# Optimization experiments

Hardware: AMD Instinct MI355X
Metric: run time of the kernel (lower is better)

Reference implementation:

```python
import jax, jax.numpy as jnp
import numpy as np

EPS = 1e-6       # eps from __init__
STEPSIZE = 1.0   # stepsize from __init__
DELTA = 0.1      # delta from __init__


def setup_inputs() -> dict:
    key = jax.random.key(0)
    k1, k2, k3 = jax.random.split(key, 3)
    N, L, H, E, M = 2, 2048, 8, 64, 64
    return {
        "queries": jax.random.normal(k1, (N, L, H, E), dtype=jnp.float32),
        "keys": jax.random.normal(k2, (N, L, H, E), dtype=jnp.float32),
        "values": jax.random.normal(k3, (N, L, H, M), dtype=jnp.float32),
        "key_lengths_mask": jnp.ones((N, L), dtype=jnp.float32),
    }


def reference(queries, keys, values, key_lengths_mask):
    # elu feature map: elu(x) + 1
    Q = jax.nn.elu(queries) + 1.0                                   # [N,L,H,E]
    K = (jax.nn.elu(keys) + 1.0) * key_lengths_mask[:, :, None, None]
    N, L, H, E = Q.shape

    # normalizer Z_t = 1 / (q_t . sum_{s<=t} k_s + eps)
    Z = 1.0 / (jnp.einsum('nlhe,nlhe->nlh', Q, jnp.cumsum(K, axis=1)) + EPS)

    # per-step outer products k_s v_s^T  (original materializes this einsum)
    KV = jnp.einsum('nlhe,nlhm->nlhem', K, values)                  # [N,L,H,E,M]

    # causal_dot_product: out_t = q_t . cumsum_s(KV)_t
    out = jnp.einsum('nlhe,nlhem->nlhm', Q, jnp.cumsum(KV, axis=1)) * Z[..., None]

    # momentum coefficients mu_j from Frobenius norms over (E,M)
    diff_norm = jnp.sqrt(jnp.sum((KV[:, 1:] - KV[:, :-1]) ** 2, axis=(3, 4)))  # [N,L-1,H]
    base_norm = jnp.sqrt(jnp.sum(KV[:, :-1] ** 2, axis=(3, 4)))
    mu = jnp.clip((1.0 - jnp.sqrt(diff_norm / base_norm)) ** 2, 0.0, 1.0 - DELTA)

    # momentum weights: a_{L-1}=1, a_j = 1 + mu_j * a_{j+1} (backward recurrence).
    # This equals both momentum_weight (cumprod-sum form) and momentum_weight_old
    # (explicit reverse loop) in the original, so Kn == Kw.
    def step(a, mu_t):
        a_new = 1.0 + mu_t * a
        return a_new, a_new

    _, a_seq = jax.lax.scan(step, jnp.ones((N, H), Q.dtype),
                            jnp.moveaxis(mu, 1, 0), reverse=True)   # [L-1,N,H]
    momentum_weight = jnp.concatenate(
        [jnp.moveaxis(a_seq, 0, 1), jnp.ones((N, 1, H), Q.dtype)], axis=1)  # [N,L,H]
    Kn = K * momentum_weight[..., None] * STEPSIZE                  # [N,L,H,E]

    return out, Kn
```

## Files before the change

### kernel.cpp

```cpp
#include <hip/hip_runtime.h>

#define N_ 2
#define L_ 2048
#define H_ 8
#define NH_ 16
#define C_ 64
#define NC_ 32
#define EPS_ 1e-6f
#define DELTA_ 0.1f

#define CHSZ 4160
#define ST_SHORTS (NH_*NC_*CHSZ)
#define KV_SHORTS (NH_*L_*64)

typedef short s8v __attribute__((ext_vector_type(8)));
typedef short s4v __attribute__((ext_vector_type(4)));
typedef float f4v __attribute__((ext_vector_type(4)));

__device__ __forceinline__ float elup1(float x){ return x>0.f ? x+1.f : __expf(x); }
__device__ __forceinline__ short f2b(float x){
  unsigned u = __float_as_uint(x);
  return (short)((u + 0x7FFFu + ((u>>16)&1u)) >> 16);
}
__device__ __forceinline__ float b2f(short s){
  return __uint_as_float(((unsigned)(unsigned short)s) << 16);
}

__global__ __launch_bounds__(512) void kA(const float* __restrict__ keys,
    const float* __restrict__ values, const float* __restrict__ mask,
    unsigned short* __restrict__ st, short* __restrict__ ktil,
    short* __restrict__ vtilT, float* __restrict__ mu)
{
  const int bid = blockIdx.x, c = bid & (NC_-1), nh = bid >> 5;
  const int n = nh >> 3, h = nh & 7, tid = threadIdx.x;

  __shared__ __attribute__((aligned(16))) short Ktb[64][72];
  __shared__ __attribute__((aligned(16))) short Vtb[80][72];
  __shared__ float prt[6][4][64];

  #pragma unroll
  for (int i = 0; i < 2; ++i) {
    const int idx4 = tid + 512*i;
    const int t = idx4 >> 4, e4 = (idx4 & 15) << 2;
    const int l = c*C_ + t;
    const size_t b = (((size_t)n*L_ + l)*H_ + h)*64 + e4;
    const float m0 = mask[n*L_ + l];
    const f4v kx = *(const f4v*)&keys[b];
    const f4v vx = *(const f4v*)&values[b];
    s4v kb4;
    #pragma unroll
    for (int j = 0; j < 4; ++j) kb4[j] = f2b(elup1(kx[j]) * m0);
    *(s4v*)&ktil[((size_t)nh*L_ + l)*64 + e4] = kb4;
    #pragma unroll
    for (int j = 0; j < 4; ++j) { Ktb[e4+j][t] = kb4[j]; Vtb[e4+j][t] = f2b(vx[j]); }
  }
  if (tid < 64) Vtb[64][tid] = (short)0x3F80;
  __syncthreads();

  {
    const int m = tid >> 3, t8 = (tid & 7) << 3;
    *(s8v*)&vtilT[((size_t)bid*64 + m)*64 + t8] = *(const s8v*)&Vtb[m][t8];
  }

  if (tid < 256) {
    const int lane = tid & 63, w = tid >> 6, r = lane & 15, g = lane >> 4;
    f4v acc[5];
    #pragma unroll
    for (int j = 0; j < 5; ++j) acc[j] = (f4v)(0.f);
    #pragma unroll
    for (int k2 = 0; k2 < 2; ++k2) {
      const s8v a = *(const s8v*)&Ktb[w*16 + r][k2*32 + g*8];
      #pragma unroll
      for (int mj = 0; mj < 5; ++mj) {
        const s8v bb = *(const s8v*)&Vtb[mj*16 + r][k2*32 + g*8];
        acc[mj] = __builtin_amdgcn_mfma_f32_16x16x32_bf16(a, bb, acc[mj], 0, 0, 0);
      }
    }
    unsigned short* sp = st + (size_t)bid*CHSZ;
    #pragma unroll
    for (int mj = 0; mj < 5; ++mj) {
      const int m = mj*16 + r;
      if (m <= 64) {
        s4v pk;
        #pragma unroll
        for (int j = 0; j < 4; ++j) pk[j] = f2b(acc[mj][j]);
        *(s4v*)&sp[(size_t)m*64 + w*16 + g*4] = pk;
      }
    }
  } else {
    const int tid2 = tid - 256;
    const int t = tid2 & 63, eq = tid2 >> 6;
    const int l = c*C_ + t;
    const int l1 = (l+1 < L_) ? l+1 : l;
    const size_t b0 = (((size_t)n*L_ + l )*H_ + h)*64 + eq*16;
    const size_t b1 = (((size_t)n*L_ + l1)*H_ + h)*64 + eq*16;
    const float m0 = mask[n*L_ + l], m1 = mask[n*L_ + l1];
    float kk0=0.f,kk1=0.f,knn=0.f,vv0=0.f,vv1=0.f,vnn=0.f;
    #pragma unroll
    for (int j = 0; j < 16; j += 4) {
      const f4v ka = *(const f4v*)&keys[b0+j];
      const f4v kc = *(const f4v*)&keys[b1+j];
      const f4v va = *(const f4v*)&values[b0+j];
      const f4v vc = *(const f4v*)&values[b1+j];
      #pragma unroll
      for (int jj = 0; jj < 4; ++jj) {
        const float k0 = elup1(ka[jj])*m0, k1 = elup1(kc[jj])*m1;
        kk0 += k0*k0; kk1 += k1*k1; knn += k0*k1;
        const float v0 = va[jj], v1 = vc[jj];
        vv0 += v0*v0; vv1 += v1*v1; vnn += v0*v1;
      }
    }
    prt[0][eq][t]=kk0; prt[1][eq][t]=kk1; prt[2][eq][t]=knn;
    prt[3][eq][t]=vv0; prt[4][eq][t]=vv1; prt[5][eq][t]=vnn;
  }
  __syncthreads();
  if (tid < 64) {
    float s[6];
    #pragma unroll
    for (int q2 = 0; q2 < 6; ++q2)
      s[q2] = prt[q2][0][tid]+prt[q2][1][tid]+prt[q2][2][tid]+prt[q2][3][tid];
    const int j = c*C_ + tid;
    float mval = 0.f;
    if (j < L_-1) {
      const float base2 = s[0]*s[3];
      float diff2 = s[1]*s[4] - 2.f*s[2]*s[5] + base2;
      diff2 = fmaxf(diff2, 0.f);
      if (base2 > 0.f) {
        const float r4 = sqrtf(sqrtf(diff2/base2));
        const float om = 1.f - r4;
        mval = fminf(om*om, 1.f - DELTA_);
      } else {
        mval = 1.f - DELTA_;
      }
    }
    mu[(size_t)nh*L_ + j] = mval;
  }
}

__global__ __launch_bounds__(256) void kBC(unsigned short* __restrict__ st,
    const float* __restrict__ mu, float* __restrict__ aw)
{
  const int bx = blockIdx.x, tid = threadIdx.x;
  if (bx < 260) {
    const int id = bx*256 + tid;
    const int nh2 = id / CHSZ;
    const int elem = id - nh2*CHSZ;
    unsigned short* base = st + (size_t)nh2*NC_*CHSZ + elem;
    unsigned short rr[NC_];
    #pragma unroll
    for (int c2 = 0; c2 < NC_; ++c2) rr[c2] = base[(size_t)c2*CHSZ];
    float acc = 0.f;
    #pragma unroll
    for (int c2 = 0; c2 < NC_; ++c2) {
      const float v = b2f((short)rr[c2]);
      base[(size_t)c2*CHSZ] = (unsigned short)f2b(acc);
      acc += v;
    }
    return;
  }
  const int nh2 = bx - 260;
  const float* mup = mu + (size_t)nh2*L_;
  float* awp = aw + (size_t)nh2*L_;
  __shared__ float Psc[256], Qsc[256];
  float lm[8];
  #pragma unroll
  for (int i = 0; i < 8; ++i) lm[i] = mup[tid*8 + i];
  float p = 1.f, q = 0.f;
  #pragma unroll
  for (int i = 7; i >= 0; --i) { q = lm[i]*q + 1.f; p *= lm[i]; }
  Psc[tid] = p; Qsc[tid] = q;
  __syncthreads();
  for (int d = 1; d < 256; d <<= 1) {
    float pr = 1.f, qr = 0.f;
    const bool has = (tid + d) < 256;
    if (has) { pr = Psc[tid+d]; qr = Qsc[tid+d]; }
    __syncthreads();
    if (has) { const float np = p*pr, nq = p*qr + q; p = np; q = nq; Psc[tid] = p; Qsc[tid] = q; }
    __syncthreads();
  }
  float x = (tid == 255) ? 1.f : Psc[tid+1] + Qsc[tid+1];
  #pragma unroll
  for (int i = 7; i >= 0; --i) { x = lm[i]*x + 1.f; awp[tid*8+i] = x; }
}

__global__ __launch_bounds__(512) void kD(const float* __restrict__ queries,
    const unsigned short* __restrict__ st, const short* __restrict__ ktil,
    const short* __restrict__ vtilT, const float* __restrict__ aw,
    float* __restrict__ out, float* __restrict__ kn)
{
  const int bid = blockIdx.x, c = bid & (NC_-1), nh = bid >> 5;
  const int n = nh >> 3, h = nh & 7, tid = threadIdx.x;
  const int lane = tid & 63, w = tid >> 6, r = lane & 15, g = lane >> 4;
  const int tt = w & 3, mg = w >> 2;

  __shared__ __attribute__((aligned(16))) short Qb[64][72];
  __shared__ __attribute__((aligned(16))) short Kb[64][72];
  __shared__ __attribute__((aligned(16))) union {
    short Pb[64][72];
    float outf[64][68];
  } U;
  __shared__ float Zl[64], al[64];

  const unsigned short* sp = st + (size_t)bid*CHSZ;
  const short* vp = vtilT + (size_t)bid*4096;
  const s8v zero8 = (s8v)(0);

  s8v sfrag[2][3], srow64[2];
  #pragma unroll
  for (int k2 = 0; k2 < 2; ++k2) {
    if (mg == 0) {
      #pragma unroll
      for (int mi = 0; mi < 3; ++mi)
        sfrag[k2][mi] = *(const s8v*)&sp[(size_t)(mi*16 + r)*64 + k2*32 + g*8];
      srow64[k2] = zero8;
    } else {
      sfrag[k2][0] = *(const s8v*)&sp[(size_t)(48 + r)*64 + k2*32 + g*8];
      srow64[k2] = (r == 0) ? *(const s8v*)&sp[(size_t)64*64 + k2*32 + g*8] : zero8;
      sfrag[k2][1] = zero8; sfrag[k2][2] = zero8;
    }
  }

  #pragma unroll
  for (int i = 0; i < 2; ++i) {
    const int idx4 = tid + 512*i;
    const int t = idx4 >> 4, e4 = (idx4 & 15) << 2;
    const int l = c*C_ + t;
    const f4v qx = __builtin_nontemporal_load(
        (const f4v*)&queries[(((size_t)n*L_ + l)*H_ + h)*64 + e4]);
    s4v qb4;
    #pragma unroll
    for (int j = 0; j < 4; ++j) qb4[j] = f2b(elup1(qx[j]));
    *(s4v*)&Qb[t][e4] = qb4;
  }
  {
    const int t = tid >> 3, e8 = (tid & 7) << 3;
    *(s8v*)&Kb[t][e8] = *(const s8v*)&ktil[((size_t)nh*L_ + c*C_ + t)*64 + e8];
  }
  if (tid < 64) al[tid] = aw[(size_t)nh*L_ + c*C_ + tid];
  __syncthreads();

  {
    const int ss = tt, th = mg;
    const bool live = (ss*16) <= (th*32 + 31);
    f4v pacc[2];
    pacc[0] = (f4v)(0.f); pacc[1] = (f4v)(0.f);
    if (live) {
      #pragma unroll
      for (int k2 = 0; k2 < 2; ++k2) {
        const s8v a = *(const s8v*)&Kb[ss*16 + r][k2*32 + g*8];
        #pragma unroll
        for (int tj2 = 0; tj2 < 2; ++tj2) {
          const s8v bb = *(const s8v*)&Qb[(th*2 + tj2)*16 + r][k2*32 + g*8];
          pacc[tj2] = __builtin_amdgcn_mfma_f32_16x16x32_bf16(a, bb, pacc[tj2], 0, 0, 0);
        }
      }
    }
    #pragma unroll
    for (int tj2 = 0; tj2 < 2; ++tj2) {
      const int t = (th*2 + tj2)*16 + r;
      s4v pk;
      #pragma unroll
      for (int j = 0; j < 4; ++j) {
        const int s2 = ss*16 + g*4 + j;
        pk[j] = (live && s2 <= t) ? f2b(pacc[tj2][j]) : (short)0;
      }
      *(s4v*)&U.Pb[t][ss*16 + g*4] = pk;
    }
  }

  s8v vfrag[2][3], vones;
  #pragma unroll
  for (int k2 = 0; k2 < 2; ++k2) {
    if (mg == 0) {
      #pragma unroll
      for (int mi = 0; mi < 3; ++mi)
        vfrag[k2][mi] = *(const s8v*)&vp[(size_t)(mi*16 + r)*64 + k2*32 + g*8];
    } else {
      vfrag[k2][0] = *(const s8v*)&vp[(size_t)(48 + r)*64 + k2*32 + g*8];
      vfrag[k2][1] = zero8; vfrag[k2][2] = zero8;
    }
  }
  {
    s8v o;
    #pragma unroll
    for (int j = 0; j < 8; ++j) o[j] = (short)0x3F80;
    vones = (r == 0 && mg == 1) ? o : zero8;
  }
  __syncthreads();

  const int nmj = (mg == 0) ? 3 : 2;
  f4v oacc[3];
  #pragma unroll
  for (int j = 0; j < 3; ++j) oacc[j] = (f4v)(0.f);
  #pragma unroll
  for (int k2 = 0; k2 < 4; ++k2) {
    const s8v a = (k2 < 2) ? *(const s8v*)&Qb[tt*16 + r][k2*32 + g*8]
                           : *(const s8v*)&U.Pb[tt*16 + r][(k2-2)*32 + g*8];
    #pragma unroll
    for (int mi = 0; mi < 3; ++mi) {
      if (mi < nmj) {
        s8v bb;
        if (k2 < 2) bb = (mg == 1 && mi == 1) ? srow64[k2] : sfrag[k2][mi];
        else        bb = (mg == 1 && mi == 1) ? vones      : vfrag[k2-2][mi];
        oacc[mi] = __builtin_amdgcn_mfma_f32_16x16x32_bf16(a, bb, oacc[mi], 0, 0, 0);
      }
    }
  }
  __syncthreads();

  if (mg == 1 && r == 0) {
    #pragma unroll
    for (int j = 0; j < 4; ++j) Zl[tt*16 + g*4 + j] = 1.f / (oacc[1][j] + EPS_);
  }
  #pragma unroll
  for (int mi = 0; mi < 3; ++mi) {
    const int mjg = mg*3 + mi;
    if (mi < nmj && mjg < 4) {
      #pragma unroll
      for (int j = 0; j < 4; ++j)
        U.outf[tt*16 + g*4 + j][mjg*16 + r] = oacc[mi][j];
    }
  }
  __syncthreads();

  #pragma unroll
  for (int i = 0; i < 2; ++i) {
    const int idx4 = tid + 512*i;
    const int t = idx4 >> 4, m4 = (idx4 & 15) << 2, l = c*C_ + t;
    f4v v = *(const f4v*)&U.outf[t][m4];
    const float z = Zl[t];
    v[0] *= z; v[1] *= z; v[2] *= z; v[3] *= z;
    __builtin_nontemporal_store(v, (f4v*)&out[(((size_t)n*L_ + l)*H_ + h)*64 + m4]);
  }
  #pragma unroll
  for (int i = 0; i < 2; ++i) {
    const int idx4 = tid + 512*i;
    const int t = idx4 >> 4, e4 = (idx4 & 15) << 2, l = c*C_ + t;
    const float a2 = al[t];
    const s4v kb4 = *(const s4v*)&Kb[t][e4];
    f4v o;
    #pragma unroll
    for (int j = 0; j < 4; ++j) o[j] = b2f(kb4[j]) * a2;
    __builtin_nontemporal_store(o, (f4v*)&kn[(((size_t)n*L_ + l)*H_ + h)*64 + e4]);
  }
}

extern "C" void kernel_launch(void* const* d_in, const int* in_sizes, int n_in,
                              void* d_out, int out_size, void* d_ws, size_t ws_size,
                              hipStream_t stream) {
  (void)in_sizes; (void)n_in; (void)out_size; (void)ws_size;
  const float* queries = (const float*)d_in[0];
  const float* keys    = (const float*)d_in[1];
  const float* values  = (const float*)d_in[2];
  const float* mask    = (const float*)d_in[3];
  float* out = (float*)d_out;
  float* kn  = out + (size_t)N_*L_*H_*64;

  unsigned short* st = (unsigned short*)d_ws;
  short* ktil = (short*)(st + ST_SHORTS);
  short* vtilT = ktil + KV_SHORTS;
  float* mu = (float*)(vtilT + KV_SHORTS);
  float* aw = mu + NH_*L_;

  hipLaunchKernelGGL(kA,  dim3(NH_*NC_), dim3(512), 0, stream,
                     keys, values, mask, st, ktil, vtilT, mu);
  hipLaunchKernelGGL(kBC, dim3(276),     dim3(256), 0, stream, st, mu, aw);
  hipLaunchKernelGGL(kD,  dim3(NH_*NC_), dim3(512), 0, stream,
                     queries, st, ktil, vtilT, aw, out, kn);
}
```

Baseline: 26.79 us.

## Fuse chunk-prefix scan and momentum-weight scan into kA via last-block counter

```diff
diff --git a/kernel.cpp b/kernel.cpp
--- a/kernel.cpp
+++ b/kernel.cpp
@@ -29,7 +29,8 @@
 __global__ __launch_bounds__(512) void kA(const float* __restrict__ keys,
     const float* __restrict__ values, const float* __restrict__ mask,
     unsigned short* __restrict__ st, short* __restrict__ ktil,
-    short* __restrict__ vtilT, float* __restrict__ mu)
+    short* __restrict__ vtilT, float* __restrict__ mu,
+    float* __restrict__ aw, unsigned* __restrict__ counters)
 {
   const int bid = blockIdx.x, c = bid & (NC_-1), nh = bid >> 5;
   const int n = nh >> 3, h = nh & 7, tid = threadIdx.x;
@@ -37,6 +38,8 @@
   __shared__ __attribute__((aligned(16))) short Ktb[64][72];
   __shared__ __attribute__((aligned(16))) short Vtb[80][72];
   __shared__ float prt[6][4][64];
+  __shared__ float Psc[512], Qsc[512];
+  __shared__ int sLast;
 
   #pragma unroll
   for (int i = 0; i < 2; ++i) {
@@ -135,52 +138,61 @@
     }
     mu[(size_t)nh*L_ + j] = mval;
   }
-}
-
-__global__ __launch_bounds__(256) void kBC(unsigned short* __restrict__ st,
-    const float* __restrict__ mu, float* __restrict__ aw)
-{
-  const int bx = blockIdx.x, tid = threadIdx.x;
-  if (bx < 260) {
-    const int id = bx*256 + tid;
-    const int nh2 = id / CHSZ;
-    const int elem = id - nh2*CHSZ;
-    unsigned short* base = st + (size_t)nh2*NC_*CHSZ + elem;
-    unsigned short rr[NC_];
-    #pragma unroll
-    for (int c2 = 0; c2 < NC_; ++c2) rr[c2] = base[(size_t)c2*CHSZ];
-    float acc = 0.f;
-    #pragma unroll
-    for (int c2 = 0; c2 < NC_; ++c2) {
-      const float v = b2f((short)rr[c2]);
-      base[(size_t)c2*CHSZ] = (unsigned short)f2b(acc);
-      acc += v;
-    }
-    return;
-  }
-  const int nh2 = bx - 260;
-  const float* mup = mu + (size_t)nh2*L_;
-  float* awp = aw + (size_t)nh2*L_;
-  __shared__ float Psc[256], Qsc[256];
-  float lm[8];
-  #pragma unroll
-  for (int i = 0; i < 8; ++i) lm[i] = mup[tid*8 + i];
-  float p = 1.f, q = 0.f;
-  #pragma unroll
-  for (int i = 7; i >= 0; --i) { q = lm[i]*q + 1.f; p *= lm[i]; }
-  Psc[tid] = p; Qsc[tid] = q;
-  __syncthreads();
-  for (int d = 1; d < 256; d <<= 1) {
-    float pr = 1.f, qr = 0.f;
-    const bool has = (tid + d) < 256;
-    if (has) { pr = Psc[tid+d]; qr = Qsc[tid+d]; }
+  __syncthreads();
+
+  if (tid == 0) {
+    __threadfence();
+    const unsigned prev = atomicAdd(&counters[nh], 1u);
+    sLast = (((prev + 1u) & (NC_-1u)) == 0u);
+  }
+  __syncthreads();
+  if (!sLast) return;
+  __threadfence();
+
+  {
+    unsigned short* basep = st + (size_t)nh*NC_*CHSZ;
+    for (int grp = tid; grp < 520; grp += 512) {
+      unsigned short* p = basep + (size_t)grp*8;
+      float acc[8];
+      #pragma unroll
+      for (int j = 0; j < 8; ++j) acc[j] = 0.f;
+      for (int ch = 0; ch < NC_; ++ch) {
+        unsigned short* qp = p + (size_t)ch*CHSZ;
+        const s8v v = *(const s8v*)qp;
+        s8v o;
+        #pragma unroll
+        for (int j = 0; j < 8; ++j) o[j] = f2b(acc[j]);
+        *(s8v*)qp = o;
+        #pragma unroll
+        for (int j = 0; j < 8; ++j) acc[j] += b2f((short)v[j]);
+      }
+    }
+  }
+
+  {
+    const float* mup = mu + (size_t)nh*L_;
+    float* awp = aw + (size_t)nh*L_;
+    float lm[4];
+    const f4v mv = *(const f4v*)&mup[tid*4];
+    #pragma unroll
+    for (int j = 0; j < 4; ++j) lm[j] = mv[j];
+    float p = 1.f, q = 0.f;
+    #pragma unroll
+    for (int i = 3; i >= 0; --i) { q = lm[i]*q + 1.f; p *= lm[i]; }
+    Psc[tid] = p; Qsc[tid] = q;
     __syncthreads();
-    if (has) { const float np = p*pr, nq = p*qr + q; p = np; q = nq; Psc[tid] = p; Qsc[tid] = q; }
-    __syncthreads();
-  }
-  float x = (tid == 255) ? 1.f : Psc[tid+1] + Qsc[tid+1];
-  #pragma unroll
-  for (int i = 7; i >= 0; --i) { x = lm[i]*x + 1.f; awp[tid*8+i] = x; }
+    for (int d = 1; d < 512; d <<= 1) {
+      float pr = 1.f, qr = 0.f;
+      const bool has = (tid + d) < 512;
+      if (has) { pr = Psc[tid+d]; qr = Qsc[tid+d]; }
+      __syncthreads();
+      if (has) { const float np = p*pr, nq = p*qr + q; p = np; q = nq; Psc[tid] = p; Qsc[tid] = q; }
+      __syncthreads();
+    }
+    float x = (tid == 511) ? 1.f : Psc[tid+1] + Qsc[tid+1];
+    #pragma unroll
+    for (int i = 3; i >= 0; --i) { x = lm[i]*x + 1.f; awp[tid*4+i] = x; }
+  }
 }
 
 __global__ __launch_bounds__(512) void kD(const float* __restrict__ queries,
@@ -361,10 +373,10 @@
   short* vtilT = ktil + KV_SHORTS;
   float* mu = (float*)(vtilT + KV_SHORTS);
   float* aw = mu + NH_*L_;
-
-  hipLaunchKernelGGL(kA,  dim3(NH_*NC_), dim3(512), 0, stream,
-                     keys, values, mask, st, ktil, vtilT, mu);
-  hipLaunchKernelGGL(kBC, dim3(276),     dim3(256), 0, stream, st, mu, aw);
-  hipLaunchKernelGGL(kD,  dim3(NH_*NC_), dim3(512), 0, stream,
+  unsigned* counters = (unsigned*)(aw + NH_*L_);
+
+  hipLaunchKernelGGL(kA, dim3(NH_*NC_), dim3(512), 0, stream,
+                     keys, values, mask, st, ktil, vtilT, mu, aw, counters);
+  hipLaunchKernelGGL(kD, dim3(NH_*NC_), dim3(512), 0, stream,
                      queries, st, ktil, vtilT, aw, out, kn);
 }
```

New measurement: 58.46 us. 2.18x slower.
